# Optimization experiments

Hardware: AMD Instinct MI355X
Metric: run time of the kernel (lower is better)

Reference implementation:

```python
import jax, jax.numpy as jnp
import numpy as np

WINDOW_SIZES = (1, 2, 3)
COV_DIM = 128
MEM_DIM = 128
BATCH = 8192


def setup_inputs() -> dict:
    rng = np.random.default_rng(0)
    sizes = rng.integers(16, 64, size=BATCH)
    total = int(sizes.sum())  # ~327k tokens
    key = jax.random.key(0)
    ks = jax.random.split(key, 10)
    s = 0.05
    inp = {
        "x": jax.random.normal(ks[0], (total, COV_DIM), jnp.float32),
        "sizes": jnp.asarray(sizes, jnp.int32),
    }
    for i, w in enumerate(WINDOW_SIZES):
        inp[f"conv_w{i}"] = jax.random.normal(ks[1 + 2 * i], (MEM_DIM, COV_DIM, w), jnp.float32) * s
        inp[f"conv_b{i}"] = jax.random.normal(ks[2 + 2 * i], (MEM_DIM,), jnp.float32) * s
    inp["lin_w"] = jax.random.normal(ks[7], (MEM_DIM, len(WINDOW_SIZES) * MEM_DIM), jnp.float32) * s
    inp["lin_b"] = jax.random.normal(ks[8], (MEM_DIM,), jnp.float32) * s
    return inp


def _temporal_conv(x, w, b):
    # x: [T, C], w: [M, C, k] -> [T-k+1, M]  (valid 1D conv, as nn.Conv1d)
    y = jax.lax.conv_general_dilated(
        x.T[None],  # [1, C, T]
        w,
        window_strides=(1,),
        padding="VALID",
        dimension_numbers=("NCH", "OIH", "NCH"),
    )[0]  # [M, L]
    return y.T + b


def _dmax(h, sizes, window_size, batch):
    # Ragged per-segment max over dim 0 of the concatenated conv output.
    # Segment i covers rows [off_i, off_i + sizes[i] - window_size + 1) where
    # off_i is the exclusive cumsum of sizes (DMax advances start_idx by sizes[i]).
    L = h.shape[0]  # total - window_size + 1
    cum = jnp.cumsum(sizes)  # [B], inclusive
    p = jnp.arange(L)
    seg = jnp.searchsorted(cum, p, side="right")  # segment owning row p
    valid = p + (window_size - 1) < cum[seg]  # within sizes[i]-w+1 prefix
    seg = jnp.where(valid, seg, batch)  # dump invalid rows in a trash segment
    return jax.ops.segment_max(h, seg, num_segments=batch + 1)[:batch]


def reference(x, sizes, conv_w0, conv_b0, conv_w1, conv_b1, conv_w2, conv_b2, lin_w, lin_b):
    batch = sizes.shape[0]
    convs = ((conv_w0, conv_b0), (conv_w1, conv_b1), (conv_w2, conv_b2))
    pools = []
    for wsz, (cw, cb) in zip(WINDOW_SIZES, convs):
        h = jax.nn.relu(_temporal_conv(x, cw, cb))  # [T-w+1, M]
        pools.append(_dmax(h, sizes, wsz, batch))  # [B, M]
    concat = jnp.concatenate(pools, axis=1)  # [B, 3M]
    return jnp.tanh(concat @ lin_w.T + lin_b)  # [B, M]
```

## Files before the change

### kernel.cpp

```cpp
#include <hip/hip_runtime.h>
#include <hip/hip_bf16.h>

typedef __bf16 bf16x8 __attribute__((ext_vector_type(8)));
typedef __bf16 bf16x4 __attribute__((ext_vector_type(4)));
typedef float  f32x4  __attribute__((ext_vector_type(4)));

#define MFMA16(a, b, c) __builtin_amdgcn_mfma_f32_16x16x32_bf16((a), (b), (c), 0, 0, 0)

__global__ void k_prep(const int* __restrict__ sizes, int* __restrict__ offsets,
                       const float* __restrict__ w0, const float* __restrict__ w1,
                       const float* __restrict__ w2, const float* __restrict__ lw,
                       __bf16* __restrict__ Wpack,
                       __bf16* __restrict__ Lhi, __bf16* __restrict__ Llo) {
  const int bid = blockIdx.x, t = threadIdx.x;
  if (bid == 240) {
    __shared__ int part[256];
    const int base = t * 32;
    int v[32];
    int s = 0;
#pragma unroll
    for (int i = 0; i < 32; ++i) { v[i] = sizes[base + i]; s += v[i]; }
    part[t] = s;
    __syncthreads();
    for (int d = 1; d < 256; d <<= 1) {
      int add = (t >= d) ? part[t - d] : 0;
      __syncthreads();
      part[t] += add;
      __syncthreads();
    }
    int run = (t == 0) ? 0 : part[t - 1];
#pragma unroll
    for (int i = 0; i < 32; ++i) { offsets[base + i] = run; run += v[i]; }
  } else if (bid < 48) {
    const int nt = bid, sl = nt >> 3, f = nt & 7;
    const int kt = t >> 6, lane = t & 63;
    const float* src; int kw, jj;
    if      (sl == 0) { src = w0; kw = 1; jj = 0; }
    else if (sl == 1) { src = w1; kw = 2; jj = 0; }
    else if (sl == 2) { src = w1; kw = 2; jj = 1; }
    else if (sl == 3) { src = w2; kw = 3; jj = 0; }
    else if (sl == 4) { src = w2; kw = 3; jj = 1; }
    else              { src = w2; kw = 3; jj = 2; }
    const int feat  = f * 16 + (lane & 15);
    const int cbase = kt * 32 + ((lane >> 4) << 3);
    __bf16* dst = Wpack + ((((nt * 4 + kt) << 6) + lane) << 3);
#pragma unroll
    for (int j = 0; j < 8; ++j)
      dst[j] = (__bf16)src[(feat * 128 + cbase + j) * kw + jj];
  } else {
    const int idx = (bid - 48) * 256 + t;
    const int j = idx & 7, lane = (idx >> 3) & 63, rest = idx >> 9;
    const int kt = rest % 12, nt = rest / 12;
    const int o = nt * 16 + (lane & 15);
    const int q = kt * 32 + ((lane >> 4) << 3) + j;
    const float v = lw[o * 384 + q];
    const __bf16 hi = (__bf16)v;
    Lhi[idx] = hi;
    Llo[idx] = (__bf16)(v - (float)hi);
  }
}

__global__ __launch_bounds__(256, 4)
void k_conv(const float* __restrict__ x, const int* __restrict__ sizes,
            const int* __restrict__ offsets,
            const float* __restrict__ cb0, const float* __restrict__ cb1,
            const float* __restrict__ cb2,
            const bf16x8* __restrict__ Wpack,
            __bf16* __restrict__ Phi, __bf16* __restrict__ Plo) {
  __shared__ __bf16 xh[66 * 136];
  const int b = blockIdx.x;
  const int s = sizes[b];
  const long off = offsets[b];
  const int t = threadIdx.x;
  const int MT = (s + 15) >> 4;

  {
    const int quads = s << 5;
    float4 v[8];
#pragma unroll
    for (int i = 0; i < 8; ++i) {
      const int qi = t + (i << 8);
      if (qi < quads) {
        const int r = qi >> 5, c = (qi & 31) << 2;
        v[i] = *(const float4*)(x + (off + r) * 128 + c);
      }
    }
#pragma unroll
    for (int i = 0; i < 8; ++i) {
      const int qi = t + (i << 8);
      if (qi < quads) {
        const int r = qi >> 5, c = (qi & 31) << 2;
        bf16x4 h; h[0] = (__bf16)v[i].x; h[1] = (__bf16)v[i].y;
                  h[2] = (__bf16)v[i].z; h[3] = (__bf16)v[i].w;
        *(bf16x4*)&xh[r * 136 + c] = h;
      }
    }
    const int zend = MT * 16 + 2;
    const int c = (t & 31) << 2;
    for (int r = s + (t >> 5); r < zend; r += 8)
      *(bf16x4*)&xh[r * 136 + c] =
          bf16x4{(__bf16)0.f, (__bf16)0.f, (__bf16)0.f, (__bf16)0.f};
  }
  __syncthreads();

  const int wid = t >> 6, lane = t & 63;
  const int lo16 = lane & 15, g16 = lane >> 4;

#pragma unroll
  for (int fi = 0; fi < 2; ++fi) {
    const int ft = wid + (fi << 2);
    const int feat = ft * 16 + lo16;

    f32x4 acc[4][3];
#pragma unroll
    for (int mt = 0; mt < 4; ++mt)
#pragma unroll
      for (int p = 0; p < 3; ++p)
        acc[mt][p] = f32x4{0.f, 0.f, 0.f, 0.f};

#pragma unroll
    for (int kt = 0; kt < 4; ++kt) {
      bf16x8 bf[6];
#pragma unroll
      for (int sl = 0; sl < 6; ++sl)
        bf[sl] = Wpack[(((sl * 8 + ft) * 4 + kt) << 6) + lane];
#pragma unroll
      for (int mt = 0; mt < 4; ++mt) {
        if (mt < MT) {
          const __bf16* ap = &xh[(mt * 16 + lo16) * 136 + kt * 32 + (g16 << 3)];
          const bf16x8 A0 = *(const bf16x8*)ap;
          const bf16x8 A1 = *(const bf16x8*)(ap + 136);
          const bf16x8 A2 = *(const bf16x8*)(ap + 272);
          acc[mt][0] = MFMA16(A0, bf[0], acc[mt][0]);
          acc[mt][1] = MFMA16(A0, bf[1], acc[mt][1]);
          acc[mt][1] = MFMA16(A1, bf[2], acc[mt][1]);
          acc[mt][2] = MFMA16(A0, bf[3], acc[mt][2]);
          acc[mt][2] = MFMA16(A1, bf[4], acc[mt][2]);
          acc[mt][2] = MFMA16(A2, bf[5], acc[mt][2]);
        }
      }
    }

    float m1 = -1e30f, m2 = -1e30f, m3 = -1e30f;
#pragma unroll
    for (int mt = 0; mt < 4; ++mt) {
      if (mt >= MT) continue;
#pragma unroll
      for (int v = 0; v < 4; ++v) {
        const int lrow = mt * 16 + g16 * 4 + v;
        if (lrow < s)     m1 = fmaxf(m1, acc[mt][0][v]);
        if (lrow < s - 1) m2 = fmaxf(m2, acc[mt][1][v]);
        if (lrow < s - 2) m3 = fmaxf(m3, acc[mt][2][v]);
      }
    }
    m1 = fmaxf(m1, __shfl_xor(m1, 16)); m1 = fmaxf(m1, __shfl_xor(m1, 32));
    m2 = fmaxf(m2, __shfl_xor(m2, 16)); m2 = fmaxf(m2, __shfl_xor(m2, 32));
    m3 = fmaxf(m3, __shfl_xor(m3, 16)); m3 = fmaxf(m3, __shfl_xor(m3, 32));
    if (g16 == 0) {
      const float p1 = fmaxf(m1 + cb0[feat], 0.f);
      const float p2 = fmaxf(m2 + cb1[feat], 0.f);
      const float p3 = fmaxf(m3 + cb2[feat], 0.f);
      const __bf16 h1 = (__bf16)p1, h2 = (__bf16)p2, h3 = (__bf16)p3;
      const long row = (long)b * 384;
      Phi[row + feat]       = h1;
      Plo[row + feat]       = (__bf16)(p1 - (float)h1);
      Phi[row + 128 + feat] = h2;
      Plo[row + 128 + feat] = (__bf16)(p2 - (float)h2);
      Phi[row + 256 + feat] = h3;
      Plo[row + 256 + feat] = (__bf16)(p3 - (float)h3);
    }
  }
}

__global__ __launch_bounds__(256, 4)
void k_lin(const __bf16* __restrict__ Phi, const __bf16* __restrict__ Plo,
           const bf16x8* __restrict__ Lhi, const bf16x8* __restrict__ Llo,
           const float* __restrict__ lb, float* __restrict__ out) {
  __shared__ __bf16 ph[16 * 392];
  __shared__ __bf16 pl[16 * 392];
  const int blk = blockIdx.x, t = threadIdx.x;
  const int mb = blk >> 1, nh = blk & 1;
  const long rbase = (long)mb * 16;
#pragma unroll
  for (int i = 0; i < 3; ++i) {
    const int ci = t + (i << 8);
    const int r = ci / 48, cc = ci % 48;
    *(int4*)&ph[r * 392 + (cc << 3)] = *(const int4*)&Phi[(rbase + r) * 384 + (cc << 3)];
    *(int4*)&pl[r * 392 + (cc << 3)] = *(const int4*)&Plo[(rbase + r) * 384 + (cc << 3)];
  }
  __syncthreads();
  const int wid = t >> 6, lane = t & 63;
  const int lo16 = lane & 15, g = lane >> 4;
  const int nt = (nh << 2) + wid;
  f32x4 ahh = f32x4{0.f, 0.f, 0.f, 0.f};
  f32x4 alh = f32x4{0.f, 0.f, 0.f, 0.f};
  f32x4 ahl = f32x4{0.f, 0.f, 0.f, 0.f};
#pragma unroll
  for (int kt = 0; kt < 12; ++kt) {
    const bf16x8 bh = Lhi[((nt * 12 + kt) << 6) + lane];
    const bf16x8 bl = Llo[((nt * 12 + kt) << 6) + lane];
    const int aoff = lo16 * 392 + kt * 32 + (g << 3);
    const bf16x8 ah = *(const bf16x8*)&ph[aoff];
    const bf16x8 al = *(const bf16x8*)&pl[aoff];
    ahh = MFMA16(ah, bh, ahh);
    alh = MFMA16(al, bh, alh);
    ahl = MFMA16(ah, bl, ahl);
  }
  const int o = (nt << 4) + lo16;
  const float bias = lb[o];
#pragma unroll
  for (int v = 0; v < 4; ++v) {
    const int r = g * 4 + v;
    const float val = ahh[v] + alh[v] + ahl[v] + bias;
    out[(rbase + r) * 128 + o] = 1.f - 2.f / (__expf(2.f * val) + 1.f);
  }
}

extern "C" void kernel_launch(void* const* d_in, const int* in_sizes, int n_in,
                              void* d_out, int out_size, void* d_ws, size_t ws_size,
                              hipStream_t stream) {
  const float* x   = (const float*)d_in[0];
  const int* sizes = (const int*)d_in[1];
  const float* w0  = (const float*)d_in[2];
  const float* cb0 = (const float*)d_in[3];
  const float* w1  = (const float*)d_in[4];
  const float* cb1 = (const float*)d_in[5];
  const float* w2  = (const float*)d_in[6];
  const float* cb2 = (const float*)d_in[7];
  const float* lw  = (const float*)d_in[8];
  const float* lb  = (const float*)d_in[9];

  char* ws = (char*)d_ws;
  size_t o = 0;
  int*    offsets = (int*)ws;                 o += 32768;
  __bf16* Wpack   = (__bf16*)(ws + o);        o += 196608;
  __bf16* Lhi     = (__bf16*)(ws + o);        o += 98304;
  __bf16* Llo     = (__bf16*)(ws + o);        o += 98304;
  __bf16* Phi     = (__bf16*)(ws + o);        o += 8192L * 384 * 2;
  __bf16* Plo     = (__bf16*)(ws + o);        o += 8192L * 384 * 2;

  k_prep<<<241, 256, 0, stream>>>(sizes, offsets, w0, w1, w2, lw, Wpack, Lhi, Llo);
  k_conv<<<8192, 256, 0, stream>>>(x, sizes, offsets, cb0, cb1, cb2,
                                   (const bf16x8*)Wpack, Phi, Plo);
  k_lin<<<1024, 256, 0, stream>>>(Phi, Plo, (const bf16x8*)Lhi,
                                  (const bf16x8*)Llo, lb, (float*)d_out);
}
```

Before: 325.0 us.

## Tile conv over flat token stream with double-buffered loads and atomic segment max

Replaces the one-block-per-segment conv with 1024 persistent blocks that walk contiguous 64-row tiles of the concatenated token stream. Each block prefetches the next tile into a second LDS buffer while computing the current one, and tracks segment boundaries per lane. Partial maxima are merged into a zeroed fp32 pool with atomicMax on the float bits, which is valid because every value is post-ReLU and so non-negative. The aim is to remove the padding waste and load imbalance of ragged segments and to overlap global loads with MFMA work, at the cost of atomics, a zeroing pass and a larger fp32 intermediate.

```diff
diff --git a/kernel.cpp b/kernel.cpp
--- a/kernel.cpp
+++ b/kernel.cpp
@@ -11,7 +11,8 @@
                        const float* __restrict__ w0, const float* __restrict__ w1,
                        const float* __restrict__ w2, const float* __restrict__ lw,
                        __bf16* __restrict__ Wpack,
-                       __bf16* __restrict__ Lhi, __bf16* __restrict__ Llo) {
+                       __bf16* __restrict__ Lhi, __bf16* __restrict__ Llo,
+                       unsigned* __restrict__ Pool) {
   const int bid = blockIdx.x, t = threadIdx.x;
   if (bid == 240) {
     __shared__ int part[256];
@@ -31,6 +32,7 @@
     int run = (t == 0) ? 0 : part[t - 1];
 #pragma unroll
     for (int i = 0; i < 32; ++i) { offsets[base + i] = run; run += v[i]; }
+    if (t == 255) offsets[8192] = run;
   } else if (bid < 48) {
     const int nt = bid, sl = nt >> 3, f = nt & 7;
     const int kt = t >> 6, lane = t & 63;
@@ -47,7 +49,7 @@
 #pragma unroll
     for (int j = 0; j < 8; ++j)
       dst[j] = (__bf16)src[(feat * 128 + cbase + j) * kw + jj];
-  } else {
+  } else if (bid < 240) {
     const int idx = (bid - 48) * 256 + t;
     const int j = idx & 7, lane = (idx >> 3) & 63, rest = idx >> 9;
     const int kt = rest % 12, nt = rest / 12;
@@ -57,77 +59,107 @@
     const __bf16 hi = (__bf16)v;
     Lhi[idx] = hi;
     Llo[idx] = (__bf16)(v - (float)hi);
+  } else {
+    int4* p = (int4*)Pool + ((bid - 241) * 1024 + t * 4);
+    const int4 z{0, 0, 0, 0};
+    p[0] = z; p[1] = z; p[2] = z; p[3] = z;
   }
 }
 
-__global__ __launch_bounds__(256, 4)
-void k_conv(const float* __restrict__ x, const int* __restrict__ sizes,
-            const int* __restrict__ offsets,
+__global__ __launch_bounds__(256, 3)
+void k_conv(const float* __restrict__ x, const int* __restrict__ offsets,
             const float* __restrict__ cb0, const float* __restrict__ cb1,
             const float* __restrict__ cb2,
             const bf16x8* __restrict__ Wpack,
-            __bf16* __restrict__ Phi, __bf16* __restrict__ Plo) {
-  __shared__ __bf16 xh[66 * 136];
-  const int b = blockIdx.x;
-  const int s = sizes[b];
-  const long off = offsets[b];
+            unsigned* __restrict__ Pool) {
+  __shared__ __align__(16) __bf16 xs[2][66 * 136];
   const int t = threadIdx.x;
-  const int MT = (s + 15) >> 4;
-
-  {
-    const int quads = s << 5;
-    float4 v[8];
-#pragma unroll
-    for (int i = 0; i < 8; ++i) {
-      const int qi = t + (i << 8);
-      if (qi < quads) {
-        const int r = qi >> 5, c = (qi & 31) << 2;
-        v[i] = *(const float4*)(x + (off + r) * 128 + c);
-      }
-    }
-#pragma unroll
-    for (int i = 0; i < 8; ++i) {
-      const int qi = t + (i << 8);
-      if (qi < quads) {
-        const int r = qi >> 5, c = (qi & 31) << 2;
-        bf16x4 h; h[0] = (__bf16)v[i].x; h[1] = (__bf16)v[i].y;
-                  h[2] = (__bf16)v[i].z; h[3] = (__bf16)v[i].w;
-        *(bf16x4*)&xh[r * 136 + c] = h;
-      }
-    }
-    const int zend = MT * 16 + 2;
-    const int c = (t & 31) << 2;
-    for (int r = s + (t >> 5); r < zend; r += 8)
-      *(bf16x4*)&xh[r * 136 + c] =
-          bf16x4{(__bf16)0.f, (__bf16)0.f, (__bf16)0.f, (__bf16)0.f};
-  }
-  __syncthreads();
-
   const int wid = t >> 6, lane = t & 63;
   const int lo16 = lane & 15, g16 = lane >> 4;
-
-#pragma unroll
-  for (int fi = 0; fi < 2; ++fi) {
-    const int ft = wid + (fi << 2);
-    const int feat = ft * 16 + lo16;
-
-    f32x4 acc[4][3];
-#pragma unroll
-    for (int mt = 0; mt < 4; ++mt)
-#pragma unroll
-      for (int p = 0; p < 3; ++p)
-        acc[mt][p] = f32x4{0.f, 0.f, 0.f, 0.f};
-
-#pragma unroll
-    for (int kt = 0; kt < 4; ++kt) {
-      bf16x8 bf[6];
-#pragma unroll
-      for (int sl = 0; sl < 6; ++sl)
-        bf[sl] = Wpack[(((sl * 8 + ft) * 4 + kt) << 6) + lane];
-#pragma unroll
-      for (int mt = 0; mt < 4; ++mt) {
-        if (mt < MT) {
-          const __bf16* ap = &xh[(mt * 16 + lo16) * 136 + kt * 32 + (g16 << 3)];
+  const int T = offsets[8192];
+  const int ntiles = (T + 63) >> 6;
+  const int per = (ntiles + 1023) >> 10;
+  const int t0 = blockIdx.x * per;
+  const int t1 = min(t0 + per, ntiles);
+  if (t0 >= t1) return;
+
+  const int feat0 = wid * 16 + lo16, feat1 = feat0 + 64;
+  const float cbv[2][3] = {{cb0[feat0], cb1[feat0], cb2[feat0]},
+                           {cb0[feat1], cb1[feat1], cb2[feat1]}};
+
+  int seg, end;
+  {
+    const int r0 = t0 * 64 + (g16 << 2);
+    int lo = 0, hi = 8192;
+    while (hi - lo > 1) {
+      const int mid = (lo + hi) >> 1;
+      if (offsets[mid] <= r0) lo = mid; else hi = mid;
+    }
+    seg = lo; end = offsets[seg + 1];
+  }
+  float pm[2][3] = {{0.f, 0.f, 0.f}, {0.f, 0.f, 0.f}};
+
+  {
+    const long tb = (long)t0 * 64;
+    float4 pa[5], pb[5]; bool pact[5];
+#pragma unroll
+    for (int k = 0; k < 5; ++k) {
+      const int u = t + (k << 8);
+      pact[k] = (k < 4 || t < 32) && (tb + (u >> 4) < T);
+      if (pact[k]) {
+        const float* p = x + (tb + (u >> 4)) * 128 + ((u & 15) << 3);
+        pa[k] = *(const float4*)p; pb[k] = *(const float4*)(p + 4);
+      }
+    }
+#pragma unroll
+    for (int k = 0; k < 5; ++k) if (pact[k]) {
+      const int u = t + (k << 8);
+      bf16x8 h;
+      h[0]=(__bf16)pa[k].x; h[1]=(__bf16)pa[k].y; h[2]=(__bf16)pa[k].z; h[3]=(__bf16)pa[k].w;
+      h[4]=(__bf16)pb[k].x; h[5]=(__bf16)pb[k].y; h[6]=(__bf16)pb[k].z; h[7]=(__bf16)pb[k].w;
+      *(bf16x8*)&xs[0][(u >> 4) * 136 + ((u & 15) << 3)] = h;
+    }
+  }
+  __syncthreads();
+
+  int cur = 0;
+  for (int tt = t0; tt < t1; ++tt) {
+    const long tb = (long)tt * 64;
+    const bool hasNext = (tt + 1 < t1);
+
+    float4 va[5], vb[5]; bool act[5] = {false, false, false, false, false};
+    if (hasNext) {
+      const long nb = tb + 64;
+#pragma unroll
+      for (int k = 0; k < 5; ++k) {
+        const int u = t + (k << 8);
+        act[k] = (k < 4 || t < 32) && (nb + (u >> 4) < T);
+        if (act[k]) {
+          const float* p = x + (nb + (u >> 4)) * 128 + ((u & 15) << 3);
+          va[k] = *(const float4*)p; vb[k] = *(const float4*)(p + 4);
+        }
+      }
+    }
+
+    const __bf16* xb = xs[cur];
+    const int sg0 = seg, en0 = end;
+#pragma unroll
+    for (int fi = 0; fi < 2; ++fi) {
+      const int ft = wid + (fi << 2);
+      f32x4 acc[4][3];
+#pragma unroll
+      for (int mt = 0; mt < 4; ++mt)
+#pragma unroll
+        for (int p = 0; p < 3; ++p) acc[mt][p] = f32x4{0.f, 0.f, 0.f, 0.f};
+#pragma unroll
+      for (int kt = 0; kt < 4; ++kt) {
+        bf16x8 bf[6];
+#pragma unroll
+        for (int sl = 0; sl < 6; ++sl)
+          bf[sl] = Wpack[(((sl * 8 + ft) * 4 + kt) << 6) + lane];
+#pragma unroll
+        for (int mt = 0; mt < 4; ++mt) {
+          const __bf16* ap = &xb[(mt * 16 + lo16) * 136 + kt * 32 + (g16 << 3)];
           const bf16x8 A0 = *(const bf16x8*)ap;
           const bf16x8 A1 = *(const bf16x8*)(ap + 136);
           const bf16x8 A2 = *(const bf16x8*)(ap + 272);
@@ -139,41 +171,57 @@
           acc[mt][2] = MFMA16(A2, bf[5], acc[mt][2]);
         }
       }
-    }
-
-    float m1 = -1e30f, m2 = -1e30f, m3 = -1e30f;
-#pragma unroll
-    for (int mt = 0; mt < 4; ++mt) {
-      if (mt >= MT) continue;
-#pragma unroll
-      for (int v = 0; v < 4; ++v) {
-        const int lrow = mt * 16 + g16 * 4 + v;
-        if (lrow < s)     m1 = fmaxf(m1, acc[mt][0][v]);
-        if (lrow < s - 1) m2 = fmaxf(m2, acc[mt][1][v]);
-        if (lrow < s - 2) m3 = fmaxf(m3, acc[mt][2][v]);
+      const int feat = fi ? feat1 : feat0;
+      int sg = sg0, en = en0;
+#pragma unroll
+      for (int mt = 0; mt < 4; ++mt)
+#pragma unroll
+        for (int v = 0; v < 4; ++v) {
+          const int r = (int)tb + mt * 16 + (g16 << 2) + v;
+          if (r < T) {
+            if (r >= en) {
+              unsigned* bp = Pool + (long)sg * 384 + feat;
+              atomicMax(bp,       __float_as_uint(pm[fi][0]));
+              atomicMax(bp + 128, __float_as_uint(pm[fi][1]));
+              atomicMax(bp + 256, __float_as_uint(pm[fi][2]));
+              pm[fi][0] = pm[fi][1] = pm[fi][2] = 0.f;
+              do { ++sg; en = offsets[sg + 1]; } while (r >= en);
+            }
+            pm[fi][0] = fmaxf(pm[fi][0], acc[mt][0][v] + cbv[fi][0]);
+            if (r + 1 < en) pm[fi][1] = fmaxf(pm[fi][1], acc[mt][1][v] + cbv[fi][1]);
+            if (r + 2 < en) pm[fi][2] = fmaxf(pm[fi][2], acc[mt][2][v] + cbv[fi][2]);
+          }
+        }
+      if (fi == 1) { seg = sg; end = en; }
+    }
+
+    if (hasNext) {
+#pragma unroll
+      for (int k = 0; k < 5; ++k) if (act[k]) {
+        const int u = t + (k << 8);
+        bf16x8 h;
+        h[0]=(__bf16)va[k].x; h[1]=(__bf16)va[k].y; h[2]=(__bf16)va[k].z; h[3]=(__bf16)va[k].w;
+        h[4]=(__bf16)vb[k].x; h[5]=(__bf16)vb[k].y; h[6]=(__bf16)vb[k].z; h[7]=(__bf16)vb[k].w;
+        *(bf16x8*)&xs[cur ^ 1][(u >> 4) * 136 + ((u & 15) << 3)] = h;
       }
-    }
-    m1 = fmaxf(m1, __shfl_xor(m1, 16)); m1 = fmaxf(m1, __shfl_xor(m1, 32));
-    m2 = fmaxf(m2, __shfl_xor(m2, 16)); m2 = fmaxf(m2, __shfl_xor(m2, 32));
-    m3 = fmaxf(m3, __shfl_xor(m3, 16)); m3 = fmaxf(m3, __shfl_xor(m3, 32));
-    if (g16 == 0) {
-      const float p1 = fmaxf(m1 + cb0[feat], 0.f);
-      const float p2 = fmaxf(m2 + cb1[feat], 0.f);
-      const float p3 = fmaxf(m3 + cb2[feat], 0.f);
-      const __bf16 h1 = (__bf16)p1, h2 = (__bf16)p2, h3 = (__bf16)p3;
-      const long row = (long)b * 384;
-      Phi[row + feat]       = h1;
-      Plo[row + feat]       = (__bf16)(p1 - (float)h1);
-      Phi[row + 128 + feat] = h2;
-      Plo[row + 128 + feat] = (__bf16)(p2 - (float)h2);
-      Phi[row + 256 + feat] = h3;
-      Plo[row + 256 + feat] = (__bf16)(p3 - (float)h3);
-    }
+      __syncthreads();
+      cur ^= 1;
+    }
+  }
+
+  {
+    unsigned* bp = Pool + (long)seg * 384;
+    atomicMax(bp + feat0,       __float_as_uint(pm[0][0]));
+    atomicMax(bp + 128 + feat0, __float_as_uint(pm[0][1]));
+    atomicMax(bp + 256 + feat0, __float_as_uint(pm[0][2]));
+    atomicMax(bp + feat1,       __float_as_uint(pm[1][0]));
+    atomicMax(bp + 128 + feat1, __float_as_uint(pm[1][1]));
+    atomicMax(bp + 256 + feat1, __float_as_uint(pm[1][2]));
   }
 }
 
 __global__ __launch_bounds__(256, 4)
-void k_lin(const __bf16* __restrict__ Phi, const __bf16* __restrict__ Plo,
+void k_lin(const float* __restrict__ Pool,
            const bf16x8* __restrict__ Lhi, const bf16x8* __restrict__ Llo,
            const float* __restrict__ lb, float* __restrict__ out) {
   __shared__ __bf16 ph[16 * 392];
@@ -182,11 +230,17 @@
   const int mb = blk >> 1, nh = blk & 1;
   const long rbase = (long)mb * 16;
 #pragma unroll
-  for (int i = 0; i < 3; ++i) {
+  for (int i = 0; i < 6; ++i) {
     const int ci = t + (i << 8);
-    const int r = ci / 48, cc = ci % 48;
-    *(int4*)&ph[r * 392 + (cc << 3)] = *(const int4*)&Phi[(rbase + r) * 384 + (cc << 3)];
-    *(int4*)&pl[r * 392 + (cc << 3)] = *(const int4*)&Plo[(rbase + r) * 384 + (cc << 3)];
+    const int r = ci / 96, c4 = ci % 96;
+    const float4 v = *(const float4*)(Pool + (rbase + r) * 384 + (c4 << 2));
+    bf16x4 h, l;
+    h[0] = (__bf16)v.x; l[0] = (__bf16)(v.x - (float)h[0]);
+    h[1] = (__bf16)v.y; l[1] = (__bf16)(v.y - (float)h[1]);
+    h[2] = (__bf16)v.z; l[2] = (__bf16)(v.z - (float)h[2]);
+    h[3] = (__bf16)v.w; l[3] = (__bf16)(v.w - (float)h[3]);
+    *(bf16x4*)&ph[r * 392 + (c4 << 2)] = h;
+    *(bf16x4*)&pl[r * 392 + (c4 << 2)] = l;
   }
   __syncthreads();
   const int wid = t >> 6, lane = t & 63;
@@ -232,16 +286,16 @@
 
   char* ws = (char*)d_ws;
   size_t o = 0;
-  int*    offsets = (int*)ws;                 o += 32768;
-  __bf16* Wpack   = (__bf16*)(ws + o);        o += 196608;
-  __bf16* Lhi     = (__bf16*)(ws + o);        o += 98304;
-  __bf16* Llo     = (__bf16*)(ws + o);        o += 98304;
-  __bf16* Phi     = (__bf16*)(ws + o);        o += 8192L * 384 * 2;
-  __bf16* Plo     = (__bf16*)(ws + o);        o += 8192L * 384 * 2;
-
-  k_prep<<<241, 256, 0, stream>>>(sizes, offsets, w0, w1, w2, lw, Wpack, Lhi, Llo);
-  k_conv<<<8192, 256, 0, stream>>>(x, sizes, offsets, cb0, cb1, cb2,
-                                   (const bf16x8*)Wpack, Phi, Plo);
-  k_lin<<<1024, 256, 0, stream>>>(Phi, Plo, (const bf16x8*)Lhi,
+  int*      offsets = (int*)ws;             o += 33280;
+  __bf16*   Wpack   = (__bf16*)(ws + o);    o += 196608;
+  __bf16*   Lhi     = (__bf16*)(ws + o);    o += 98304;
+  __bf16*   Llo     = (__bf16*)(ws + o);    o += 98304;
+  unsigned* Pool    = (unsigned*)(ws + o);  o += 8192L * 384 * 4;
+
+  k_prep<<<1009, 256, 0, stream>>>(sizes, offsets, w0, w1, w2, lw,
+                                   Wpack, Lhi, Llo, Pool);
+  k_conv<<<1024, 256, 0, stream>>>(x, offsets, cb0, cb1, cb2,
+                                   (const bf16x8*)Wpack, Pool);
+  k_lin<<<1024, 256, 0, stream>>>((const float*)Pool, (const bf16x8*)Lhi,
                                   (const bf16x8*)Llo, lb, (float*)d_out);
 }
```

New measurement: 762.5 us. 135% more time.
